# Kernel tuning notes

Measured on AMD Instinct MI355X. Metric: run time of the kernel, lower is better.

The kernel has to match this reference:

```python
import jax, jax.numpy as jnp
import numpy as np

B, C, H, W = 8, 256, 64, 64
CK = 64  # C // k with k=4


def setup_inputs() -> dict:
    key = jax.random.key(0)
    ks = jax.random.split(key, 5)
    s = 1.0 / np.sqrt(C)
    return {
        "x": jax.random.normal(ks[0], (B, C, H, W), dtype=jnp.float32),
        "wq": jax.random.normal(ks[1], (CK, C), dtype=jnp.float32) * s,
        "bq": jnp.zeros((CK,), dtype=jnp.float32),
        "wk": jax.random.normal(ks[2], (CK, C), dtype=jnp.float32) * s,
        "bk": jnp.zeros((CK,), dtype=jnp.float32),
        "wv": jax.random.normal(ks[3], (C, C), dtype=jnp.float32) * s,
        "bv": jnp.zeros((C,), dtype=jnp.float32),
        "wg": jax.random.normal(ks[4], (C, C), dtype=jnp.float32) * s,
        "bg": jnp.zeros((C,), dtype=jnp.float32),
    }


def reference(x, wq, bq, wk, bk, wv, bv, wg, bg):
    b, c, h, w = x.shape
    n = h * w
    xf = x.reshape(b, c, n)  # [B, C, N]
    # 1x1 convs are channel-wise matmuls
    q = jnp.einsum('oc,bcn->bon', wq, xf) + bq[None, :, None]  # [B, Ck, N]
    k = jnp.einsum('oc,bcn->bon', wk, xf) + bk[None, :, None]  # [B, Ck, N]
    v = jnp.einsum('oc,bcn->bon', wv, xf) + bv[None, :, None]  # [B, C, N]
    # energy[b,i,j] = q[b,:,i] . k[b,:,j]
    energy = jnp.einsum('bci,bcj->bij', q, k)  # [B, N, N]
    energy = jax.nn.elu(energy) / n
    out = jnp.einsum('bcn,bnj->bcj', v, energy).reshape(b, c, h, w)
    out = jnp.einsum('oc,bchw->bohw', wg, out) + bg[None, :, None, None]
    return out
```

## Files before the change

### kernel.cpp

```cpp
#include <hip/hip_runtime.h>
#include <math.h>

#define BATCH 8
#define CH    256
#define NPIX  4096
#define CKDIM 64

typedef __attribute__((ext_vector_type(8))) short short8;
typedef __attribute__((ext_vector_type(4))) float f32x4;

#define MFMA16x16(a, b, c) __builtin_amdgcn_mfma_f32_16x16x32_bf16((a), (b), (c), 0, 0, 0)

__device__ __forceinline__ unsigned short f2bf(float f) {
    union { float f; unsigned int u; } v; v.f = f;
    unsigned int u = v.u;
    u += 0x7fffu + ((u >> 16) & 1u);
    return (unsigned short)(u >> 16);
}

__global__ void prep_kernel(const float* __restrict__ wq, const float* __restrict__ bq,
                            const float* __restrict__ wk, const float* __restrict__ bk,
                            const float* __restrict__ wv, const float* __restrict__ bv,
                            const float* __restrict__ wg,
                            unsigned short* __restrict__ W_all, float* __restrict__ bias_all) {
    int o = blockIdx.x;
    int c = threadIdx.x;
    if (o < 64) {
        W_all[o * CH + c] = f2bf(wq[o * CH + c]);
        if (c == 0) bias_all[o] = bq[o];
    } else if (o < 128) {
        int oo = o - 64;
        W_all[o * CH + c] = f2bf(wk[oo * CH + c]);
        if (c == 0) bias_all[o] = bk[oo];
    } else {
        int oo = o - 128;
        float acc = 0.f;
        for (int m = 0; m < CH; ++m)
            acc += wg[oo * CH + m] * wv[m * CH + c];
        W_all[o * CH + c] = f2bf(acc);
        if (c == 0) {
            float b = 0.f;
            for (int m = 0; m < CH; ++m) b += wg[oo * CH + m] * bv[m];
            bias_all[o] = b;
        }
    }
}

__global__ void xpose_kernel(const float* __restrict__ x, unsigned short* __restrict__ xt) {
    __shared__ float Tl[64][65];
    int n0 = blockIdx.x * 64;
    int c0 = blockIdx.y * 64;
    int b  = blockIdx.z;
    int tid = threadIdx.x;

#pragma unroll
    for (int r = 0; r < 4; ++r) {
        int f  = r * 256 + tid;
        int c  = f >> 4;
        int n4 = f & 15;
        float4 v = *(const float4*)(x + ((size_t)b * CH + c0 + c) * NPIX + n0 + n4 * 4);
        Tl[n4 * 4 + 0][c] = v.x;
        Tl[n4 * 4 + 1][c] = v.y;
        Tl[n4 * 4 + 2][c] = v.z;
        Tl[n4 * 4 + 3][c] = v.w;
    }
    __syncthreads();
#pragma unroll
    for (int r = 0; r < 2; ++r) {
        int f    = r * 256 + tid;
        int nrow = f >> 3;
        int c8   = f & 7;
        unsigned int pk[4];
#pragma unroll
        for (int p = 0; p < 4; ++p) {
            unsigned int lo = f2bf(Tl[nrow][c8 * 8 + p * 2 + 0]);
            unsigned int hi = f2bf(Tl[nrow][c8 * 8 + p * 2 + 1]);
            pk[p] = lo | (hi << 16);
        }
        *(uint4*)(xt + ((size_t)b * NPIX + n0 + nrow) * CH + c0 + c8 * 8) = *(uint4*)pk;
    }
}

__global__ void qkv_mfma(const unsigned short* __restrict__ xt,
                         const unsigned short* __restrict__ W_all,
                         const float* __restrict__ bias_all,
                         unsigned short* __restrict__ qk, unsigned short* __restrict__ vp) {
    __shared__ __align__(16) unsigned short Xl[64][264];

    int n0   = blockIdx.x * 64;
    int b    = blockIdx.y;
    int tid  = threadIdx.x;
    int lane = tid & 63;
    int w    = tid >> 6;
    int col  = lane & 15;
    int quad = lane >> 4;

#pragma unroll
    for (int r = 0; r < 8; ++r) {
        int f   = r * 256 + tid;
        int row = f >> 5;
        int c8  = f & 31;
        *(uint4*)&Xl[row][c8 * 8] = *(const uint4*)(xt + ((size_t)b * NPIX + n0 + row) * CH + c8 * 8);
    }
    __syncthreads();

#pragma unroll
    for (int og = 0; og < 6; ++og) {
        int o0 = og * 64;
        const unsigned short* Arow = W_all + (size_t)(o0 + w * 16 + col) * CH + quad * 8;

        f32x4 acc[4];
#pragma unroll
        for (int t = 0; t < 4; ++t) acc[t] = (f32x4){0.f, 0.f, 0.f, 0.f};

#pragma unroll
        for (int kc = 0; kc < 8; ++kc) {
            short8 a = *(const short8*)(Arow + kc * 32);
#pragma unroll
            for (int nt = 0; nt < 4; ++nt) {
                short8 bb = *(const short8*)&Xl[nt * 16 + col][kc * 32 + quad * 8];
                acc[nt] = MFMA16x16(a, bb, acc[nt]);
            }
        }

        float4 bias = *(const float4*)(bias_all + o0 + w * 16 + quad * 4);
        float bs[4] = {bias.x, bias.y, bias.z, bias.w};

        if (og < 2) {
#pragma unroll
            for (int nt = 0; nt < 4; ++nt) {
                int n = n0 + nt * 16 + col;
                unsigned int pk[2];
#pragma unroll
                for (int p = 0; p < 2; ++p) {
                    unsigned int lo = f2bf(acc[nt][p * 2 + 0] + bs[p * 2 + 0]);
                    unsigned int hi = f2bf(acc[nt][p * 2 + 1] + bs[p * 2 + 1]);
                    pk[p] = lo | (hi << 16);
                }
                *(uint2*)(qk + ((size_t)b * NPIX + n) * 128 + o0 + w * 16 + quad * 4) = *(uint2*)pk;
            }
        } else {
#pragma unroll
            for (int nt = 0; nt < 4; ++nt) {
                int n = n0 + nt * 16 + col;
#pragma unroll
                for (int r = 0; r < 4; ++r) {
                    int oo = o0 - 128 + w * 16 + quad * 4 + r;
                    vp[((size_t)b * CH + oo) * NPIX + n] = f2bf(acc[nt][r] + bs[r]);
                }
            }
        }
    }
}

#define LPK 72
__global__ __launch_bounds__(512, 4)
void attn_v6(const unsigned short* __restrict__ qk,
             const unsigned short* __restrict__ vp,
             const float* __restrict__ bg, float* __restrict__ out) {
    __shared__ __align__(16) unsigned short Qt[64][LPK];
    __shared__ __align__(16) unsigned short St[64][LPK];

    int lin  = blockIdx.y * gridDim.x + blockIdx.x;
    int b    = lin & 7;
    int j0   = (lin >> 3) * 64;
    int tid  = threadIdx.x;
    int lane = tid & 63;
    int w    = tid >> 6;
    int col  = lane & 15;
    int quad = lane >> 4;

    int tjA = w & 3;
    int tiP = (w >> 2) * 2;

    short8 bK[2];
#pragma unroll
    for (int ks = 0; ks < 2; ++ks)
        bK[ks] = *(const short8*)(qk + ((size_t)b * NPIX + j0 + tjA * 16 + col) * 128 + 64 + ks * 32 + quad * 8);

    f32x4 acc[2][4];
#pragma unroll
    for (int ot = 0; ot < 2; ++ot)
#pragma unroll
        for (int tj = 0; tj < 4; ++tj) acc[ot][tj] = (f32x4){0.f, 0.f, 0.f, 0.f};

    int qrow = tid >> 3, q8 = tid & 7;
    const unsigned short* Qsrc = qk + ((size_t)b * NPIX + qrow) * 128 + q8 * 8;
    const unsigned short* Vsrc[2];
#pragma unroll
    for (int ot = 0; ot < 2; ++ot)
        Vsrc[ot] = vp + ((size_t)b * CH + (w * 2 + ot) * 16 + col) * NPIX + quad * 8;

    uint4 qr = *(const uint4*)Qsrc;
    short8 vb[2][2];
#pragma unroll
    for (int ot = 0; ot < 2; ++ot)
#pragma unroll
        for (int ks = 0; ks < 2; ++ks)
            vb[ot][ks] = *(const short8*)(Vsrc[ot] + ks * 32);

    const float invN = 1.f / (float)NPIX;

    for (int i0 = 0; i0 < NPIX; i0 += 64) {
        *(uint4*)&Qt[qrow][q8 * 8] = qr;

        int inext = (i0 + 64) & (NPIX - 1);
        uint4 qr_n = *(const uint4*)(Qsrc + (size_t)inext * 128);
        short8 vb_n[2][2];
#pragma unroll
        for (int ot = 0; ot < 2; ++ot)
#pragma unroll
            for (int ks = 0; ks < 2; ++ks)
                vb_n[ot][ks] = *(const short8*)(Vsrc[ot] + inext + ks * 32);

        __syncthreads();

#pragma unroll
        for (int t = 0; t < 2; ++t) {
            int ti = tiP + t;
            short8 a0 = *(const short8*)&Qt[ti * 16 + col][quad * 8];
            short8 a1 = *(const short8*)&Qt[ti * 16 + col][32 + quad * 8];
            f32x4 s = (f32x4){0.f, 0.f, 0.f, 0.f};
            s = MFMA16x16(a0, bK[0], s);
            s = MFMA16x16(a1, bK[1], s);
            unsigned int pk2[2];
#pragma unroll
            for (int pp = 0; pp < 2; ++pp) {
                float e0 = s[pp * 2 + 0];
                float e1 = s[pp * 2 + 1];
                float g0 = __expf(e0) - 1.f;
                float g1 = __expf(e1) - 1.f;
                e0 = (e0 > 0.f) ? e0 : g0;
                e1 = (e1 > 0.f) ? e1 : g1;
                e0 *= invN;
                e1 *= invN;
                unsigned int rpk;
                asm("v_cvt_pk_bf16_f32 %0, %1, %2" : "=v"(rpk) : "v"(e0), "v"(e1));
                pk2[pp] = rpk;
            }
            *(uint2*)&St[tjA * 16 + col][ti * 16 + quad * 4] = *(uint2*)pk2;
        }
        __syncthreads();

#pragma unroll
        for (int ks = 0; ks < 2; ++ks) {
            short8 sb[4];
#pragma unroll
            for (int tj = 0; tj < 4; ++tj)
                sb[tj] = *(const short8*)&St[tj * 16 + col][ks * 32 + quad * 8];
            __builtin_amdgcn_s_setprio(1);
#pragma unroll
            for (int ot = 0; ot < 2; ++ot)
#pragma unroll
                for (int tj = 0; tj < 4; ++tj)
                    acc[ot][tj] = MFMA16x16(sb[tj], vb[ot][ks], acc[ot][tj]);
            __builtin_amdgcn_s_setprio(0);
        }

        qr = qr_n;
#pragma unroll
        for (int ot = 0; ot < 2; ++ot)
#pragma unroll
            for (int ks = 0; ks < 2; ++ks)
                vb[ot][ks] = vb_n[ot][ks];
    }

#pragma unroll
    for (int ot = 0; ot < 2; ++ot) {
        int o = (w * 2 + ot) * 16 + col;
        float bgv = bg[o];
#pragma unroll
        for (int tj = 0; tj < 4; ++tj) {
            int j = j0 + tj * 16 + quad * 4;
            float4 st;
            st.x = acc[ot][tj][0] + bgv;
            st.y = acc[ot][tj][1] + bgv;
            st.z = acc[ot][tj][2] + bgv;
            st.w = acc[ot][tj][3] + bgv;
            *(float4*)&out[((size_t)b * CH + o) * NPIX + j] = st;
        }
    }
}

extern "C" void kernel_launch(void* const* d_in, const int* in_sizes, int n_in,
                              void* d_out, int out_size, void* d_ws, size_t ws_size,
                              hipStream_t stream) {
    const float* x  = (const float*)d_in[0];
    const float* wq = (const float*)d_in[1];
    const float* bq = (const float*)d_in[2];
    const float* wk = (const float*)d_in[3];
    const float* bk = (const float*)d_in[4];
    const float* wv = (const float*)d_in[5];
    const float* bv = (const float*)d_in[6];
    const float* wg = (const float*)d_in[7];
    const float* bg = (const float*)d_in[8];
    float* out = (float*)d_out;

    unsigned short* W_all = (unsigned short*)d_ws;
    float* bias_all = (float*)(W_all + 384 * 256);
    unsigned short* xt = (unsigned short*)(bias_all + 384);
    unsigned short* qk = xt + (size_t)BATCH * NPIX * CH;
    unsigned short* vp = qk + (size_t)BATCH * NPIX * 128;

    prep_kernel<<<dim3(384), dim3(256), 0, stream>>>(wq, bq, wk, bk, wv, bv, wg, W_all, bias_all);
    xpose_kernel<<<dim3(NPIX / 64, CH / 64, BATCH), dim3(256), 0, stream>>>(x, xt);
    qkv_mfma<<<dim3(NPIX / 64, BATCH), dim3(256), 0, stream>>>(xt, W_all, bias_all, qk, vp);
    attn_v6<<<dim3(NPIX / 64, BATCH), dim3(512), 0, stream>>>(qk, vp, bg, out);
}
```

Baseline: 266.0 us.

## Fuse transpose into QKV projection kernel and speed up weight prep

Folds the fp32-to-bf16 transpose of x into the QKV MFMA kernel. Each block now loads four 64-channel slices of x, transposes them through shared memory and writes straight into the bf16 tile it consumes, which removes the intermediate xt buffer's global write and read plus one kernel launch. Prep also caches the wg row in shared memory and splits the Wg*Wv dot product into four partial accumulators. In exchange the fused kernel uses more shared memory, adds serial sync steps before the matmul, and carries a launch-bounds hint.

```diff
diff --git a/kernel.cpp b/kernel.cpp
--- a/kernel.cpp
+++ b/kernel.cpp
@@ -33,58 +33,33 @@
         W_all[o * CH + c] = f2bf(wk[oo * CH + c]);
         if (c == 0) bias_all[o] = bk[oo];
     } else {
+        __shared__ float wgr[CH];
         int oo = o - 128;
-        float acc = 0.f;
-        for (int m = 0; m < CH; ++m)
-            acc += wg[oo * CH + m] * wv[m * CH + c];
-        W_all[o * CH + c] = f2bf(acc);
+        wgr[c] = wg[oo * CH + c];
+        __syncthreads();
+        float a0 = 0.f, a1 = 0.f, a2 = 0.f, a3 = 0.f;
+#pragma unroll 4
+        for (int m = 0; m < CH; m += 4) {
+            a0 += wgr[m + 0] * wv[(m + 0) * CH + c];
+            a1 += wgr[m + 1] * wv[(m + 1) * CH + c];
+            a2 += wgr[m + 2] * wv[(m + 2) * CH + c];
+            a3 += wgr[m + 3] * wv[(m + 3) * CH + c];
+        }
+        W_all[o * CH + c] = f2bf((a0 + a1) + (a2 + a3));
         if (c == 0) {
             float b = 0.f;
-            for (int m = 0; m < CH; ++m) b += wg[oo * CH + m] * bv[m];
+            for (int m = 0; m < CH; ++m) b += wgr[m] * bv[m];
             bias_all[o] = b;
         }
     }
 }
 
-__global__ void xpose_kernel(const float* __restrict__ x, unsigned short* __restrict__ xt) {
+__global__ __launch_bounds__(256, 2)
+void qkvf_mfma(const float* __restrict__ x,
+               const unsigned short* __restrict__ W_all,
+               const float* __restrict__ bias_all,
+               unsigned short* __restrict__ qk, unsigned short* __restrict__ vp) {
     __shared__ float Tl[64][65];
-    int n0 = blockIdx.x * 64;
-    int c0 = blockIdx.y * 64;
-    int b  = blockIdx.z;
-    int tid = threadIdx.x;
-
-#pragma unroll
-    for (int r = 0; r < 4; ++r) {
-        int f  = r * 256 + tid;
-        int c  = f >> 4;
-        int n4 = f & 15;
-        float4 v = *(const float4*)(x + ((size_t)b * CH + c0 + c) * NPIX + n0 + n4 * 4);
-        Tl[n4 * 4 + 0][c] = v.x;
-        Tl[n4 * 4 + 1][c] = v.y;
-        Tl[n4 * 4 + 2][c] = v.z;
-        Tl[n4 * 4 + 3][c] = v.w;
-    }
-    __syncthreads();
-#pragma unroll
-    for (int r = 0; r < 2; ++r) {
-        int f    = r * 256 + tid;
-        int nrow = f >> 3;
-        int c8   = f & 7;
-        unsigned int pk[4];
-#pragma unroll
-        for (int p = 0; p < 4; ++p) {
-            unsigned int lo = f2bf(Tl[nrow][c8 * 8 + p * 2 + 0]);
-            unsigned int hi = f2bf(Tl[nrow][c8 * 8 + p * 2 + 1]);
-            pk[p] = lo | (hi << 16);
-        }
-        *(uint4*)(xt + ((size_t)b * NPIX + n0 + nrow) * CH + c0 + c8 * 8) = *(uint4*)pk;
-    }
-}
-
-__global__ void qkv_mfma(const unsigned short* __restrict__ xt,
-                         const unsigned short* __restrict__ W_all,
-                         const float* __restrict__ bias_all,
-                         unsigned short* __restrict__ qk, unsigned short* __restrict__ vp) {
     __shared__ __align__(16) unsigned short Xl[64][264];
 
     int n0   = blockIdx.x * 64;
@@ -95,12 +70,34 @@
     int col  = lane & 15;
     int quad = lane >> 4;
 
-#pragma unroll
-    for (int r = 0; r < 8; ++r) {
-        int f   = r * 256 + tid;
-        int row = f >> 5;
-        int c8  = f & 31;
-        *(uint4*)&Xl[row][c8 * 8] = *(const uint4*)(xt + ((size_t)b * NPIX + n0 + row) * CH + c8 * 8);
+    for (int c0 = 0; c0 < CH; c0 += 64) {
+        if (c0) __syncthreads();
+#pragma unroll
+        for (int r = 0; r < 4; ++r) {
+            int f  = r * 256 + tid;
+            int c  = f >> 4;
+            int n4 = f & 15;
+            float4 v = *(const float4*)(x + ((size_t)b * CH + c0 + c) * NPIX + n0 + n4 * 4);
+            Tl[n4 * 4 + 0][c] = v.x;
+            Tl[n4 * 4 + 1][c] = v.y;
+            Tl[n4 * 4 + 2][c] = v.z;
+            Tl[n4 * 4 + 3][c] = v.w;
+        }
+        __syncthreads();
+#pragma unroll
+        for (int r = 0; r < 2; ++r) {
+            int f    = r * 256 + tid;
+            int nrow = f >> 3;
+            int c8   = f & 7;
+            unsigned int pk[4];
+#pragma unroll
+            for (int p = 0; p < 4; ++p) {
+                unsigned int lo = f2bf(Tl[nrow][c8 * 8 + p * 2 + 0]);
+                unsigned int hi = f2bf(Tl[nrow][c8 * 8 + p * 2 + 1]);
+                pk[p] = lo | (hi << 16);
+            }
+            *(uint4*)&Xl[nrow][c0 + c8 * 8] = *(uint4*)pk;
+        }
     }
     __syncthreads();
 
@@ -298,12 +295,10 @@
 
     unsigned short* W_all = (unsigned short*)d_ws;
     float* bias_all = (float*)(W_all + 384 * 256);
-    unsigned short* xt = (unsigned short*)(bias_all + 384);
-    unsigned short* qk = xt + (size_t)BATCH * NPIX * CH;
+    unsigned short* qk = (unsigned short*)(bias_all + 384);
     unsigned short* vp = qk + (size_t)BATCH * NPIX * 128;
 
     prep_kernel<<<dim3(384), dim3(256), 0, stream>>>(wq, bq, wk, bk, wv, bv, wg, W_all, bias_all);
-    xpose_kernel<<<dim3(NPIX / 64, CH / 64, BATCH), dim3(256), 0, stream>>>(x, xt);
-    qkv_mfma<<<dim3(NPIX / 64, BATCH), dim3(256), 0, stream>>>(xt, W_all, bias_all, qk, vp);
+    qkvf_mfma<<<dim3(NPIX / 64, BATCH), dim3(256), 0, stream>>>(x, W_all, bias_all, qk, vp);
     attn_v6<<<dim3(NPIX / 64, BATCH), dim3(512), 0, stream>>>(qk, vp, bg, out);
 }
```

New measurement: 257.5 us. 1.03x faster.
